# Kernel optimization log

Measured on AMD Instinct MI355X. Metric: run time of the kernel, lower is better.

The kernel has to match this reference:

```python
import jax, jax.numpy as jnp
import numpy as np

WS = 4            # window_size
C = 192           # dim
NH = 6            # num_heads
HD = C // NH      # head_dim
HID = 384         # mlp hidden = int(dim * mlp_ratio)
EPS = 1e-5


def _rel_pos_index(ws):
    coords = np.stack(np.meshgrid(np.arange(ws), np.arange(ws), np.arange(ws), indexing='ij'))  # [3,ws,ws,ws]
    cf = coords.reshape(3, -1)                                # [3, N]
    rel = cf[:, :, None] - cf[:, None, :]                     # [3, N, N]
    rel = rel.transpose(1, 2, 0)                              # [N, N, 3]
    rel += ws - 1
    rel[:, :, 0] *= (2 * ws - 1) * (2 * ws - 1)
    rel[:, :, 1] *= 2 * ws - 1
    return jnp.asarray(rel.sum(-1), dtype=jnp.int32)          # [N, N]

REL_IDX = _rel_pos_index(WS)


def setup_inputs() -> dict:
    key = jax.random.key(0)
    ks = jax.random.split(key, 20)
    s = 0.02
    B, Dd, Hh, Ww = 2, 48, 48, 48
    L = Dd * Hh * Ww
    tbl = (2 * WS - 1) ** 3
    return {
        'x': jax.random.normal(ks[0], (B, L, C), jnp.float32),
        'D': Dd, 'H': Hh, 'W': Ww,
        'ln1_g': jnp.ones((C,), jnp.float32), 'ln1_b': jnp.zeros((C,), jnp.float32),
        'ln2_g': jnp.ones((C,), jnp.float32), 'ln2_b': jnp.zeros((C,), jnp.float32),
        'qkv_w': jax.random.normal(ks[1], (C, 3 * C), jnp.float32) * s,
        'qkv_b': jnp.zeros((3 * C,), jnp.float32),
        'rpb_table': jax.random.normal(ks[2], (tbl, NH), jnp.float32) * s,
        'proj_w': jax.random.normal(ks[3], (C, C), jnp.float32) * s,
        'proj_b': jnp.zeros((C,), jnp.float32),
        'fc1_w': jax.random.normal(ks[4], (C, HID), jnp.float32) * s,
        'fc1_b': jnp.zeros((HID,), jnp.float32),
        'dw_w': jax.random.normal(ks[5], (HID, 1, 3, 3, 3), jnp.float32) * s,
        'dw_b': jnp.zeros((HID,), jnp.float32),
        'bn_g': jnp.ones((HID,), jnp.float32), 'bn_b': jnp.zeros((HID,), jnp.float32),
        'bn_mean': jnp.zeros((HID,), jnp.float32), 'bn_var': jnp.ones((HID,), jnp.float32),
        'fc2_w': jax.random.normal(ks[6], (HID, C), jnp.float32) * s,
        'fc2_b': jnp.zeros((C,), jnp.float32),
    }


def _ln(x, g, b):
    m = jnp.mean(x, -1, keepdims=True)
    v = jnp.mean((x - m) ** 2, -1, keepdims=True)
    return (x - m) * jax.lax.rsqrt(v + EPS) * g + b


def _window_attn(xw, qkv_w, qkv_b, rpb_table, proj_w, proj_b):
    # xw: [nW, N, C]
    nW, N, _ = xw.shape
    qkv = (xw @ qkv_w + qkv_b).reshape(nW, N, 3, NH, HD)
    q, k, v = qkv[:, :, 0], qkv[:, :, 1], qkv[:, :, 2]   # [nW, N, NH, HD]
    scale = HD ** -0.5
    attn = jnp.einsum('wnhd,wmhd->whnm', q * scale, k)    # [nW, NH, N, N]
    bias = rpb_table[REL_IDX]                              # [N, N, NH]
    attn = attn + jnp.transpose(bias, (2, 0, 1))[None]
    attn = jax.nn.softmax(attn, axis=-1)
    out = jnp.einsum('whnm,wmhd->wnhd', attn, v).reshape(nW, N, C)
    return out @ proj_w + proj_b


def reference(x, D, H, W, ln1_g, ln1_b, ln2_g, ln2_b, qkv_w, qkv_b, rpb_table,
              proj_w, proj_b, fc1_w, fc1_b, dw_w, dw_b, bn_g, bn_b, bn_mean,
              bn_var, fc2_w, fc2_b):
    B, L, _ = x.shape
    shortcut = x
    # --- windowed attention ---
    xs = _ln(x, ln1_g, ln1_b).reshape(B, D, H, W, C)
    # D,H,W divisible by WS -> no padding
    xs = xs.reshape(B, D // WS, WS, H // WS, WS, W // WS, WS, C)
    xw = jnp.transpose(xs, (0, 1, 3, 5, 2, 4, 6, 7)).reshape(-1, WS ** 3, C)
    aw = _window_attn(xw, qkv_w, qkv_b, rpb_table, proj_w, proj_b)
    aw = aw.reshape(B, D // WS, H // WS, W // WS, WS, WS, WS, C)
    xr = jnp.transpose(aw, (0, 1, 4, 2, 5, 3, 6, 7)).reshape(B, L, C)
    x = shortcut + xr
    # --- efficient MLP: fc1 -> dwconv3d -> BN(eval) -> GELU -> fc2 ---
    y = _ln(x, ln2_g, ln2_b)
    h = y @ fc1_w + fc1_b                                  # [B, L, HID]
    hs = jnp.transpose(h, (0, 2, 1)).reshape(B, HID, D, H, W)
    hs = jax.lax.conv_general_dilated(
        hs, dw_w, window_strides=(1, 1, 1), padding='SAME',
        feature_group_count=HID,
        dimension_numbers=('NCDHW', 'OIDHW', 'NCDHW')) + dw_b[None, :, None, None, None]
    hs = (hs - bn_mean[None, :, None, None, None]) * jax.lax.rsqrt(
        bn_var[None, :, None, None, None] + EPS) * bn_g[None, :, None, None, None] + bn_b[None, :, None, None, None]
    h = jnp.transpose(hs.reshape(B, HID, L), (0, 2, 1))
    h = jax.nn.gelu(h, approximate=False)
    return x + (h @ fc2_w + fc2_b)
```

## Files before the change

kernel.cpp:

```cpp
#include <hip/hip_runtime.h>

typedef __bf16 bf16;
typedef __bf16 bf16x8 __attribute__((ext_vector_type(8)));
typedef float f32x4 __attribute__((ext_vector_type(4)));
typedef float f32x2 __attribute__((ext_vector_type(2)));

#define L_TOT 110592
#define TOKS  221184
#define NWIN  3456

static __device__ __forceinline__ f32x4 mfma16(bf16x8 a, bf16x8 b, f32x4 c) {
    return __builtin_amdgcn_mfma_f32_16x16x32_bf16(a, b, c, 0, 0, 0);
}
static __device__ __forceinline__ bf16x8 ld8(const bf16* p) { return *(const bf16x8*)p; }
static __device__ __forceinline__ f32x2 pkfma(float w, f32x2 v, f32x2 c) {
    return __builtin_elementwise_fma((f32x2){w, w}, v, c);
}

__global__ void wt_frag(const float* __restrict__ src, bf16* __restrict__ dst, int K, int N) {
    int i = blockIdx.x * 256 + threadIdx.x;
    if (i >= K * N) return;
    int kw = i & 31, col = (i >> 5) & 63, rest = i >> 11;
    int nks = K >> 5;
    int ks = rest % nks, chunk = rest / nks;
    int n = chunk * 64 + col, k = ks * 32 + kw;
    dst[i] = (bf16)src[k * N + n];
}

__global__ void bias6_build(const float* __restrict__ rpb, float* __restrict__ bias6) {
    int i = blockIdx.x * 256 + threadIdx.x;
    if (i >= 6 * 64 * 64) return;
    int h = i >> 12, n = (i >> 6) & 63, m = i & 63;
    int r0 = (n >> 4) - (m >> 4) + 3;
    int r1 = ((n >> 2) & 3) - ((m >> 2) & 3) + 3;
    int r2 = (n & 3) - (m & 3) + 3;
    bias6[i] = rpb[(r0 * 49 + r1 * 7 + r2) * 6 + h];
}

__global__ void ln1_window(const float* __restrict__ x, const float* __restrict__ g,
                           const float* __restrict__ bt, bf16* __restrict__ xw) {
    int wave = threadIdx.x >> 6, lane = threadIdx.x & 63;
    int t = blockIdx.x * 4 + wave;
    const float* row = x + (long)t * 192;
    float v0 = row[lane], v1 = row[lane + 64], v2 = row[lane + 128];
    float s = v0 + v1 + v2;
    #pragma unroll
    for (int m = 1; m < 64; m <<= 1) s += __shfl_xor(s, m);
    float mu = s * (1.0f / 192.0f);
    float d0 = v0 - mu, d1 = v1 - mu, d2 = v2 - mu;
    float q = d0 * d0 + d1 * d1 + d2 * d2;
    #pragma unroll
    for (int m = 1; m < 64; m <<= 1) q += __shfl_xor(q, m);
    float r = rsqrtf(q * (1.0f / 192.0f) + 1e-5f);
    int b = t / L_TOT, l = t - b * L_TOT;
    int dz = l / 2304, rem = l - dz * 2304;
    int hy = rem / 48, wx = rem - hy * 48;
    int w = ((b * 12 + (dz >> 2)) * 12 + (hy >> 2)) * 12 + (wx >> 2);
    int n = (dz & 3) * 16 + (hy & 3) * 4 + (wx & 3);
    bf16* o = xw + (long)w * 12288 + (lane >> 5) * 2048 + n * 32 + (lane & 31);
    o[0]    = (bf16)(d0 * r * g[lane]       + bt[lane]);
    o[4096] = (bf16)(d1 * r * g[lane + 64]  + bt[lane + 64]);
    o[8192] = (bf16)(d2 * r * g[lane + 128] + bt[lane + 128]);
}

__global__ void ln2_kernel(const bf16* __restrict__ in, const float* __restrict__ g,
                           const float* __restrict__ bt, bf16* __restrict__ y) {
    int wave = threadIdx.x >> 6, lane = threadIdx.x & 63;
    long t = blockIdx.x * 4 + wave;
    const bf16* row = in + t * 192;
    float v0 = (float)row[lane], v1 = (float)row[lane + 64], v2 = (float)row[lane + 128];
    float s = v0 + v1 + v2;
    #pragma unroll
    for (int m = 1; m < 64; m <<= 1) s += __shfl_xor(s, m);
    float mu = s * (1.0f / 192.0f);
    float d0 = v0 - mu, d1 = v1 - mu, d2 = v2 - mu;
    float q = d0 * d0 + d1 * d1 + d2 * d2;
    #pragma unroll
    for (int m = 1; m < 64; m <<= 1) q += __shfl_xor(q, m);
    float r = rsqrtf(q * (1.0f / 192.0f) + 1e-5f);
    bf16* o = y + (t >> 6) * 12288 + (lane >> 5) * 2048 + (t & 63) * 32 + (lane & 31);
    o[0]    = (bf16)(d0 * r * g[lane]       + bt[lane]);
    o[4096] = (bf16)(d1 * r * g[lane + 64]  + bt[lane + 64]);
    o[8192] = (bf16)(d2 * r * g[lane + 128] + bt[lane + 128]);
}

__global__ __launch_bounds__(256) void gemm_qkv(
    const bf16* __restrict__ xw, const bf16* __restrict__ wt,
    const float* __restrict__ bqkv,
    bf16* __restrict__ qb, bf16* __restrict__ kb_, bf16* __restrict__ vtb) {
    int m0 = blockIdx.x * 128;
    int w0 = m0 >> 6;
    int wid = threadIdx.x >> 6, lane = threadIdx.x & 63;
    int wr = wid >> 1, wc = wid & 1;
    int lo = lane & 15, hi = lane >> 4;
    f32x4 zf = {0.f, 0.f, 0.f, 0.f};

    const bf16* Ab = xw + (long)(w0 + wr) * 12288 + (lo * 32 + hi * 8);
    bf16x8 a[4][6];
    #pragma unroll
    for (int ti = 0; ti < 4; ++ti)
        #pragma unroll
        for (int ks = 0; ks < 6; ++ks)
            a[ti][ks] = ld8(Ab + ks * 2048 + ti * 512);

    #pragma unroll
    for (int nc = 0; nc < 9; ++nc) {
        int sect = nc / 3;
        int cb0 = (nc - sect * 3) * 64;
        f32x4 acc[4][2];
        #pragma unroll
        for (int i = 0; i < 4; ++i) { acc[i][0] = zf; acc[i][1] = zf; }
        const bf16* Bb = wt + (long)nc * 12288 + (wc * 32 + lo) * 32 + hi * 8;
        #pragma unroll
        for (int ks = 0; ks < 6; ++ks) {
            bf16x8 b0 = ld8(Bb + ks * 2048);
            bf16x8 b1 = ld8(Bb + ks * 2048 + 512);
            #pragma unroll
            for (int ti = 0; ti < 4; ++ti) {
                acc[ti][0] = mfma16(a[ti][ks], b0, acc[ti][0]);
                acc[ti][1] = mfma16(a[ti][ks], b1, acc[ti][1]);
            }
        }
        #pragma unroll
        for (int ti = 0; ti < 4; ++ti)
            #pragma unroll
            for (int j = 0; j < 4; ++j) {
                int trow = m0 + wr * 64 + ti * 16 + hi * 4 + j;
                int w = trow >> 6, n = trow & 63;
                #pragma unroll
                for (int tj = 0; tj < 2; ++tj) {
                    int cw = cb0 + wc * 32 + tj * 16 + lo;
                    int h = cw >> 5, d = cw & 31;
                    float val = acc[ti][tj][j] + bqkv[sect * 192 + cw];
                    long wh = (long)(w * 6 + h);
                    if (sect == 0)       qb[(wh * 64 + n) * 32 + d] = (bf16)(val * 0.17677669529663687f);
                    else if (sect == 1)  kb_[(wh * 64 + n) * 32 + d] = (bf16)val;
                    else                 vtb[(wh * 32 + d) * 64 + n] = (bf16)val;
                }
            }
    }
}

__global__ __launch_bounds__(384) void attn_light(
    const bf16* __restrict__ qb, const bf16* __restrict__ kb_,
    const bf16* __restrict__ vtb, const float* __restrict__ bias6,
    bf16* __restrict__ aw) {
    __shared__ char p_smem[6 * 8192];
    int w = blockIdx.x;
    int h = threadIdx.x >> 6;
    int lane = threadIdx.x & 63;
    int lo = lane & 15, hi = lane >> 4;
    char* ph = p_smem + h * 8192;
    long wh = (long)(w * 6 + h);
    f32x4 zf = {0.f, 0.f, 0.f, 0.f};

    bf16x8 qa[4], kb[4];
    #pragma unroll
    for (int ti = 0; ti < 4; ++ti) qa[ti] = ld8(qb  + (wh * 64 + ti * 16 + lo) * 32 + hi * 8);
    #pragma unroll
    for (int tj = 0; tj < 4; ++tj) kb[tj] = ld8(kb_ + (wh * 64 + tj * 16 + lo) * 32 + hi * 8);
    f32x4 s[4][4];
    #pragma unroll
    for (int ti = 0; ti < 4; ++ti)
        #pragma unroll
        for (int tj = 0; tj < 4; ++tj)
            s[ti][tj] = mfma16(qa[ti], kb[tj], zf);

    const float* bh = bias6 + h * 4096;
    #pragma unroll
    for (int ti = 0; ti < 4; ++ti)
        #pragma unroll
        for (int j = 0; j < 4; ++j) {
            int rr = ti * 16 + hi * 4 + j;
            float ev[4];
            #pragma unroll
            for (int tj = 0; tj < 4; ++tj) s[ti][tj][j] += bh[rr * 64 + tj * 16 + lo];
            float mx = fmaxf(fmaxf(s[ti][0][j], s[ti][1][j]), fmaxf(s[ti][2][j], s[ti][3][j]));
            #pragma unroll
            for (int m = 1; m < 16; m <<= 1) mx = fmaxf(mx, __shfl_xor(mx, m));
            float sum = 0.f;
            #pragma unroll
            for (int tj = 0; tj < 4; ++tj) { ev[tj] = __expf(s[ti][tj][j] - mx); sum += ev[tj]; }
            #pragma unroll
            for (int m = 1; m < 16; m <<= 1) sum += __shfl_xor(sum, m);
            float inv = 1.0f / sum;
            #pragma unroll
            for (int tj = 0; tj < 4; ++tj) {
                int byte = ((rr * 64 + tj * 16 + lo) * 2) ^ ((rr & 7) << 4);
                *(bf16*)(ph + byte) = (bf16)(ev[tj] * inv);
            }
        }

    f32x4 o[4][2];
    #pragma unroll
    for (int i = 0; i < 4; ++i) { o[i][0] = zf; o[i][1] = zf; }
    #pragma unroll
    for (int ks2 = 0; ks2 < 2; ++ks2) {
        bf16x8 pa[4], vb[2];
        #pragma unroll
        for (int ti = 0; ti < 4; ++ti) {
            int row = ti * 16 + lo;
            pa[ti] = *(const bf16x8*)(ph + ((row * 128 + ks2 * 64 + hi * 16) ^ ((row & 7) << 4)));
        }
        #pragma unroll
        for (int td = 0; td < 2; ++td)
            vb[td] = ld8(vtb + (wh * 32 + td * 16 + lo) * 64 + ks2 * 32 + hi * 8);
        #pragma unroll
        for (int ti = 0; ti < 4; ++ti)
            #pragma unroll
            for (int td = 0; td < 2; ++td)
                o[ti][td] = mfma16(pa[ti], vb[td], o[ti][td]);
    }
    bf16* orow = aw + wh * 2048;
    #pragma unroll
    for (int ti = 0; ti < 4; ++ti)
        #pragma unroll
        for (int td = 0; td < 2; ++td)
            #pragma unroll
            for (int j = 0; j < 4; ++j)
                orow[(ti * 16 + hi * 4 + j) * 32 + td * 16 + lo] = (bf16)o[ti][td][j];
}

__global__ __launch_bounds__(256) void gemm_proj(
    const bf16* __restrict__ aw, const bf16* __restrict__ wt,
    const float* __restrict__ bias, const float* __restrict__ x,
    bf16* __restrict__ out1) {
    int m0 = blockIdx.x * 128;
    int w0 = m0 >> 6;
    int wid = threadIdx.x >> 6, lane = threadIdx.x & 63;
    int wr = wid >> 1, wc = wid & 1;
    int lo = lane & 15, hi = lane >> 4;
    f32x4 zf = {0.f, 0.f, 0.f, 0.f};

    const bf16* Ab = aw + (long)(w0 + wr) * 12288 + (lo * 32 + hi * 8);
    bf16x8 a[4][6];
    #pragma unroll
    for (int ti = 0; ti < 4; ++ti)
        #pragma unroll
        for (int ks = 0; ks < 6; ++ks)
            a[ti][ks] = ld8(Ab + ks * 2048 + ti * 512);

    #pragma unroll
    for (int nc = 0; nc < 3; ++nc) {
        f32x4 acc[4][2];
        #pragma unroll
        for (int i = 0; i < 4; ++i) { acc[i][0] = zf; acc[i][1] = zf; }
        const bf16* Bb = wt + (long)nc * 12288 + (wc * 32 + lo) * 32 + hi * 8;
        #pragma unroll
        for (int ks = 0; ks < 6; ++ks) {
            bf16x8 b0 = ld8(Bb + ks * 2048);
            bf16x8 b1 = ld8(Bb + ks * 2048 + 512);
            #pragma unroll
            for (int ti = 0; ti < 4; ++ti) {
                acc[ti][0] = mfma16(a[ti][ks], b0, acc[ti][0]);
                acc[ti][1] = mfma16(a[ti][ks], b1, acc[ti][1]);
            }
        }
        #pragma unroll
        for (int ti = 0; ti < 4; ++ti)
            #pragma unroll
            for (int j = 0; j < 4; ++j) {
                int trow = m0 + wr * 64 + ti * 16 + hi * 4 + j;
                int wv = trow >> 6, n = trow & 63;
                int bb = wv / 1728; int rem = wv - bb * 1728;
                int dq = rem / 144; int rem2 = rem - dq * 144;
                int hq = rem2 / 12; int wq = rem2 - hq * 12;
                int l = (dq * 4 + (n >> 4)) * 2304 + (hq * 4 + ((n >> 2) & 3)) * 48 + (wq * 4 + (n & 3));
                long base = ((long)bb * L_TOT + l) * 192;
                #pragma unroll
                for (int tj = 0; tj < 2; ++tj) {
                    int col = nc * 64 + wc * 32 + tj * 16 + lo;
                    out1[base + col] = (bf16)(x[base + col] + acc[ti][tj][j] + bias[col]);
                }
            }
    }
}

__global__ __launch_bounds__(256) void gemm_fc1(
    const bf16* __restrict__ y, const bf16* __restrict__ wt,
    const float* __restrict__ bias, bf16* __restrict__ h_t) {
    __shared__ bf16 tl[64][136];
    int m0 = blockIdx.x * 128;
    int c0 = m0 >> 6;
    int wid = threadIdx.x >> 6, lane = threadIdx.x & 63;
    int wr = wid >> 1, wc = wid & 1;
    int lo = lane & 15, hi = lane >> 4;
    f32x4 zf = {0.f, 0.f, 0.f, 0.f};
    int bb = m0 / L_TOT; int l0 = m0 - bb * L_TOT;
    int col = threadIdx.x >> 2, seg = threadIdx.x & 3;

    const bf16* Ab = y + (long)(c0 + wr) * 12288 + (lo * 32 + hi * 8);
    bf16x8 a[4][6];
    #pragma unroll
    for (int ti = 0; ti < 4; ++ti)
        #pragma unroll
        for (int ks = 0; ks < 6; ++ks)
            a[ti][ks] = ld8(Ab + ks * 2048 + ti * 512);

    #pragma unroll
    for (int nc = 0; nc < 6; ++nc) {
        f32x4 acc[4][2];
        #pragma unroll
        for (int i = 0; i < 4; ++i) { acc[i][0] = zf; acc[i][1] = zf; }
        const bf16* Bb = wt + (long)nc * 12288 + (wc * 32 + lo) * 32 + hi * 8;
        #pragma unroll
        for (int ks = 0; ks < 6; ++ks) {
            bf16x8 b0 = ld8(Bb + ks * 2048);
            bf16x8 b1 = ld8(Bb + ks * 2048 + 512);
            #pragma unroll
            for (int ti = 0; ti < 4; ++ti) {
                acc[ti][0] = mfma16(a[ti][ks], b0, acc[ti][0]);
                acc[ti][1] = mfma16(a[ti][ks], b1, acc[ti][1]);
            }
        }
        if (nc) __syncthreads();
        #pragma unroll
        for (int ti = 0; ti < 4; ++ti)
            #pragma unroll
            for (int tj = 0; tj < 2; ++tj)
                #pragma unroll
                for (int j = 0; j < 4; ++j) {
                    int rl = wr * 64 + ti * 16 + hi * 4 + j;
                    int cl = wc * 32 + tj * 16 + lo;
                    tl[cl][rl] = (bf16)(acc[ti][tj][j] + bias[nc * 64 + cl]);
                }
        __syncthreads();
        bf16* dst = h_t + ((long)bb * 384 + nc * 64 + col) * L_TOT + l0 + seg * 32;
        #pragma unroll
        for (int i8 = 0; i8 < 4; ++i8)
            *(bf16x8*)(dst + i8 * 8) = *(const bf16x8*)(&tl[col][seg * 32 + i8 * 8]);
    }
}

__global__ __launch_bounds__(320) void dwconv_bn_gelu(
    const bf16* __restrict__ h_t, const float* __restrict__ wconv,
    const float* __restrict__ cb, const float* __restrict__ bng,
    const float* __restrict__ bnb, const float* __restrict__ bnm,
    const float* __restrict__ bnv, bf16* __restrict__ g_t) {
    __shared__ __align__(16) bf16 tile[289 * 56];
    int blk = blockIdx.x;
    int bb = blk / 4608; int rem = blk - bb * 4608;
    int ch = rem / 12; int zb = rem - ch * 12; int z0 = zb * 4;
    const bf16* src = h_t + ((long)bb * 384 + ch) * L_TOT;

    uint4 zv = make_uint4(0u, 0u, 0u, 0u);
    for (int i = threadIdx.x; i < 295; i += 320) {
        int e = (i < 7) ? i * 8 : ((i - 7 + 1) * 56 + 48);
        *(uint4*)(tile + e) = zv;
    }
    for (int c = threadIdx.x; c < 1728; c += 320) {
        int zi = c / 288; int rc = c - zi * 288;
        int r = rc / 6; int cx8 = rc - r * 6;
        int gz = z0 - 1 + zi;
        uint4 val = zv;
        if (gz >= 0 && gz < 48) val = *(const uint4*)(src + (long)gz * 2304 + r * 48 + cx8 * 8);
        *(uint4*)(tile + (1 + zi * 48 + r) * 56 + cx8 * 8) = val;
    }
    float wgt[27];
    #pragma unroll
    for (int i = 0; i < 27; ++i) wgt[i] = wconv[ch * 27 + i];
    float scale = bng[ch] * rsqrtf(bnv[ch] + 1e-5f);
    float shift = bnb[ch] - bnm[ch] * scale;
    float cbias = cb[ch];
    __syncthreads();

    if (threadIdx.x < 288) {
        int y = threadIdx.x / 6, cx = threadIdx.x - y * 6, x0 = cx * 8;
        __builtin_assume(y < 48);
        bool up_ok = (y > 0), dn_ok = (y < 47);
        bf16* dstc = g_t + ((long)bb * 384 + ch) * L_TOT + (long)z0 * 2304 + y * 48 + x0;
        f32x2 accp[4][4];
        #pragma unroll
        for (int p = 0; p < 4; ++p)
            #pragma unroll
            for (int i = 0; i < 4; ++i) accp[p][i] = (f32x2){0.f, 0.f};

        #pragma unroll
        for (int zi = 0; zi < 6; ++zi) {
            const bf16* plane = tile + (1 + zi * 48) * 56;
            #pragma unroll
            for (int dy = 0; dy < 3; ++dy) {
                bool ok = (dy == 1) || (dy == 0 ? up_ok : dn_ok);
                if (ok) {
                    const bf16* rp = plane + (y + dy - 1) * 56 + x0;
                    bf16x8 mv = ld8(rp);
                    float d[8];
                    #pragma unroll
                    for (int i = 0; i < 8; ++i) d[i] = (float)mv[i];
                    float hl = (float)rp[-1];
                    float hr = (float)rp[8];
                    f32x2 E[5], O[4];
                    E[0] = (f32x2){hl,  d[0]};
                    E[1] = (f32x2){d[1], d[2]};
                    E[2] = (f32x2){d[3], d[4]};
                    E[3] = (f32x2){d[5], d[6]};
                    E[4] = (f32x2){d[7], hr};
                    O[0] = (f32x2){d[0], d[1]};
                    O[1] = (f32x2){d[2], d[3]};
                    O[2] = (f32x2){d[4], d[5]};
                    O[3] = (f32x2){d[6], d[7]};
                    #pragma unroll
                    for (int dz = 0; dz < 3; ++dz) {
                        int p = zi - dz;
                        if (p >= 0 && p <= 3) {
                            float w0 = wgt[dz * 9 + dy * 3 + 0];
                            float w1 = wgt[dz * 9 + dy * 3 + 1];
                            float w2 = wgt[dz * 9 + dy * 3 + 2];
                            #pragma unroll
                            for (int i = 0; i < 4; ++i)
                                accp[p][i] = pkfma(w0, E[i], pkfma(w1, O[i], pkfma(w2, E[i + 1], accp[p][i])));
                        }
                    }
                }
            }
            if (zi >= 2) {
                int p = zi - 2;
                bf16x8 ov;
                #pragma unroll
                for (int k = 0; k < 8; ++k) {
                    float v = accp[p][k >> 1][k & 1] + cbias;
                    v = fmaf(v, scale, shift);
                    float v2 = v * v;
                    float u2 = v * fmaf(v2, 0.0713548162726f, 1.5957691216057308f);
                    float e  = __expf(u2);
                    float q  = __builtin_amdgcn_rcpf(e + 1.0f);
                    ov[k] = (bf16)(v - v * q);
                }
                *(bf16x8*)(dstc + p * 2304) = ov;
            }
        }
    }
}

__global__ __launch_bounds__(256) void gemm_fc2(
    const bf16* __restrict__ g_t, const bf16* __restrict__ wt,
    const float* __restrict__ bias, const bf16* __restrict__ out1,
    float* __restrict__ out) {
    __shared__ bf16 As[2][4096];
    int m0 = blockIdx.x * 64;
    int wc = threadIdx.x >> 6, lane = threadIdx.x & 63;
    int lo = lane & 15, hi = lane >> 4;
    int bb = m0 / L_TOT, l0 = m0 - bb * L_TOT;
    f32x4 zf = {0.f, 0.f, 0.f, 0.f};
    f32x4 acc[3][4];
    #pragma unroll
    for (int tj = 0; tj < 3; ++tj)
        #pragma unroll
        for (int ti = 0; ti < 4; ++ti) acc[tj][ti] = zf;

    int sch = threadIdx.x >> 3;
    int seg = threadIdx.x & 7;
    const bf16* srcb = g_t + ((long)bb * 384 + sch) * L_TOT + l0 + seg * 8;

    bf16x8 r[2][2];
    #pragma unroll
    for (int p = 0; p < 2; ++p) r[0][p] = ld8(srcb + (long)(p * 32) * L_TOT);
    #pragma unroll
    for (int p = 0; p < 2; ++p)
        #pragma unroll
        for (int i = 0; i < 8; ++i)
            As[0][(seg * 8 + i) * 64 + ((p * 32 + sch) ^ (((seg ^ i) & 7) << 3))] = r[0][p][i];
    #pragma unroll
    for (int p = 0; p < 2; ++p) r[0][p] = ld8(srcb + (long)(64 + p * 32) * L_TOT);
    #pragma unroll
    for (int p = 0; p < 2; ++p) r[1][p] = ld8(srcb + (long)(128 + p * 32) * L_TOT);

    float res[3][4][4];
    #pragma unroll
    for (int tj = 0; tj < 3; ++tj)
        #pragma unroll
        for (int ti = 0; ti < 4; ++ti)
            #pragma unroll
            for (int j = 0; j < 4; ++j) {
                long trow = m0 + ti * 16 + hi * 4 + j;
                res[tj][ti][j] = (float)out1[trow * 192 + wc * 48 + tj * 16 + lo];
            }
    __syncthreads();

    #pragma unroll
    for (int t = 0; t < 6; ++t) {
        const bf16* Ac = As[t & 1];
        #pragma unroll
        for (int ksin = 0; ksin < 2; ++ksin) {
            bf16x8 a[4];
            #pragma unroll
            for (int ti = 0; ti < 4; ++ti) {
                int rr = ti * 16 + lo;
                int S = ((rr >> 3) ^ rr) & 7;
                a[ti] = *(const bf16x8*)&Ac[rr * 64 + ((ksin * 32 + hi * 8) ^ (S << 3))];
            }
            #pragma unroll
            for (int tj = 0; tj < 3; ++tj) {
                int cstart = wc * 48 + tj * 16;
                bf16x8 b0 = ld8(wt + ((long)((cstart >> 6) * 12 + t * 2 + ksin) * 64 + (cstart & 63) + lo) * 32 + hi * 8);
                #pragma unroll
                for (int ti = 0; ti < 4; ++ti)
                    acc[tj][ti] = mfma16(a[ti], b0, acc[tj][ti]);
            }
        }
        if (t < 5) {
            bf16* An = As[(t + 1) & 1];
            #pragma unroll
            for (int p = 0; p < 2; ++p)
                #pragma unroll
                for (int i = 0; i < 8; ++i)
                    An[(seg * 8 + i) * 64 + ((p * 32 + sch) ^ (((seg ^ i) & 7) << 3))] = r[t & 1][p][i];
        }
        if (t < 3) {
            #pragma unroll
            for (int p = 0; p < 2; ++p)
                r[t & 1][p] = ld8(srcb + (long)((t + 3) * 64 + p * 32) * L_TOT);
        }
        __syncthreads();
    }
    #pragma unroll
    for (int tj = 0; tj < 3; ++tj)
        #pragma unroll
        for (int ti = 0; ti < 4; ++ti)
            #pragma unroll
            for (int j = 0; j < 4; ++j) {
                long trow = m0 + ti * 16 + hi * 4 + j;
                int col = wc * 48 + tj * 16 + lo;
                out[trow * 192 + col] = res[tj][ti][j] + acc[tj][ti][j] + bias[col];
            }
}

extern "C" void kernel_launch(void* const* d_in, const int* in_sizes, int n_in,
                              void* d_out, int out_size, void* d_ws, size_t ws_size,
                              hipStream_t stream) {
    (void)in_sizes; (void)n_in; (void)out_size; (void)ws_size;
    const float* x     = (const float*)d_in[0];
    const float* ln1g  = (const float*)d_in[4];
    const float* ln1b  = (const float*)d_in[5];
    const float* ln2g  = (const float*)d_in[6];
    const float* ln2b  = (const float*)d_in[7];
    const float* qkvw  = (const float*)d_in[8];
    const float* qkvb  = (const float*)d_in[9];
    const float* rpb   = (const float*)d_in[10];
    const float* projw = (const float*)d_in[11];
    const float* projb = (const float*)d_in[12];
    const float* fc1w  = (const float*)d_in[13];
    const float* fc1b  = (const float*)d_in[14];
    const float* dww   = (const float*)d_in[15];
    const float* dwb   = (const float*)d_in[16];
    const float* bng   = (const float*)d_in[17];
    const float* bnb   = (const float*)d_in[18];
    const float* bnm   = (const float*)d_in[19];
    const float* bnv   = (const float*)d_in[20];
    const float* fc2w  = (const float*)d_in[21];
    const float* fc2b  = (const float*)d_in[22];
    float* out = (float*)d_out;

    char* ws = (char*)d_ws;
    size_t o = 0;
    bf16*  out1 = (bf16*)(ws + o);
    bf16*  vt_buf = (bf16*)(ws + o + 84934656); o += 169869312;
    bf16*  h_t  = (bf16*)(ws + o); o += 169869312;
    bf16*  region1 = (bf16*)(ws + o); o += 169869312;
    bf16*  xw  = region1;
    bf16*  aw  = region1 + 42467328;
    bf16*  yb  = region1;
    bf16*  g_t = region1;
    bf16*  qkvwt  = (bf16*)(ws + o); o += 221184;
    bf16*  projwt = (bf16*)(ws + o); o += 73728;
    bf16*  fc1wt  = (bf16*)(ws + o); o += 147456;
    bf16*  fc2wt  = (bf16*)(ws + o); o += 147456;
    float* bias6  = (float*)(ws + o); o += 98304;

    bf16* q_buf  = h_t;
    bf16* k_buf  = h_t + 42467328;

    wt_frag<<<(110592 + 255) / 256, 256, 0, stream>>>(qkvw, qkvwt, 192, 576);
    wt_frag<<<(36864 + 255) / 256, 256, 0, stream>>>(projw, projwt, 192, 192);
    wt_frag<<<(73728 + 255) / 256, 256, 0, stream>>>(fc1w, fc1wt, 192, 384);
    wt_frag<<<(73728 + 255) / 256, 256, 0, stream>>>(fc2w, fc2wt, 384, 192);
    bias6_build<<<96, 256, 0, stream>>>(rpb, bias6);

    ln1_window<<<55296, 256, 0, stream>>>(x, ln1g, ln1b, xw);
    gemm_qkv<<<1728, 256, 0, stream>>>(xw, qkvwt, qkvb, q_buf, k_buf, vt_buf);
    attn_light<<<NWIN, 384, 0, stream>>>(q_buf, k_buf, vt_buf, bias6, aw);
    gemm_proj<<<1728, 256, 0, stream>>>(aw, projwt, projb, x, out1);
    ln2_kernel<<<55296, 256, 0, stream>>>(out1, ln2g, ln2b, yb);
    gemm_fc1<<<1728, 256, 0, stream>>>(yb, fc1wt, fc1b, h_t);
    dwconv_bn_gelu<<<9216, 320, 0, stream>>>(h_t, dww, dwb, bng, bnb, bnm, bnv, g_t);
    gemm_fc2<<<3456, 256, 0, stream>>>(g_t, fc2wt, fc2b, out1, out);
}
```

Measured before the change: 739.7 us.

## Pad dwconv smem rows to 60, load per-thread rows, use scalar FMAs

The depthwise conv kernel's shared tile row stride changes from 56 to 60 bf16 elements, with reads and writes split into 8-byte halves, presumably to reduce LDS bank conflicts. The tile is now filled so each active thread loads its own row segment for all six z planes, and only the halo words are zeroed. Packed f32x2 FMAs are replaced by scalar fmaf over a 10-element window, which removes the register shuffling that built the packed pairs but may issue more instructions. The GELU sigmoid's constants are pre-scaled by log2(e) so exp2f can replace __expf.

```diff
diff --git a/kernel.cpp b/kernel.cpp
--- a/kernel.cpp
+++ b/kernel.cpp
@@ -2,8 +2,8 @@
 
 typedef __bf16 bf16;
 typedef __bf16 bf16x8 __attribute__((ext_vector_type(8)));
+typedef __bf16 bf16x4 __attribute__((ext_vector_type(4)));
 typedef float f32x4 __attribute__((ext_vector_type(4)));
-typedef float f32x2 __attribute__((ext_vector_type(2)));
 
 #define L_TOT 110592
 #define TOKS  221184
@@ -13,9 +13,6 @@
     return __builtin_amdgcn_mfma_f32_16x16x32_bf16(a, b, c, 0, 0, 0);
 }
 static __device__ __forceinline__ bf16x8 ld8(const bf16* p) { return *(const bf16x8*)p; }
-static __device__ __forceinline__ f32x2 pkfma(float w, f32x2 v, f32x2 c) {
-    return __builtin_elementwise_fma((f32x2){w, w}, v, c);
-}
 
 __global__ void wt_frag(const float* __restrict__ src, bf16* __restrict__ dst, int K, int N) {
     int i = blockIdx.x * 256 + threadIdx.x;
@@ -337,24 +334,31 @@
     const float* __restrict__ cb, const float* __restrict__ bng,
     const float* __restrict__ bnb, const float* __restrict__ bnm,
     const float* __restrict__ bnv, bf16* __restrict__ g_t) {
-    __shared__ __align__(16) bf16 tile[289 * 56];
+    __shared__ __align__(16) bf16 tile[289 * 60];
     int blk = blockIdx.x;
     int bb = blk / 4608; int rem = blk - bb * 4608;
     int ch = rem / 12; int zb = rem - ch * 12; int z0 = zb * 4;
     const bf16* src = h_t + ((long)bb * 384 + ch) * L_TOT;
 
-    uint4 zv = make_uint4(0u, 0u, 0u, 0u);
-    for (int i = threadIdx.x; i < 295; i += 320) {
-        int e = (i < 7) ? i * 8 : ((i - 7 + 1) * 56 + 48);
-        *(uint4*)(tile + e) = zv;
-    }
-    for (int c = threadIdx.x; c < 1728; c += 320) {
-        int zi = c / 288; int rc = c - zi * 288;
-        int r = rc / 6; int cx8 = rc - r * 6;
-        int gz = z0 - 1 + zi;
-        uint4 val = zv;
-        if (gz >= 0 && gz < 48) val = *(const uint4*)(src + (long)gz * 2304 + r * 48 + cx8 * 8);
-        *(uint4*)(tile + (1 + zi * 48 + r) * 56 + cx8 * 8) = val;
+    int y = threadIdx.x / 6, cx = threadIdx.x - y * 6, x0 = cx * 8;
+    bool active = threadIdx.x < 288;
+
+    uint2 z2 = make_uint2(0u, 0u);
+    for (int i = threadIdx.x; i < 15; i += 320) *(uint2*)(tile + i * 4) = z2;
+    for (int i = threadIdx.x; i < 576; i += 320) {
+        int r = (i >> 1) + 1;
+        *(unsigned*)(tile + r * 60 + ((i & 1) ? 58 : 48)) = 0u;
+    }
+    if (active) {
+        #pragma unroll
+        for (int zi = 0; zi < 6; ++zi) {
+            int gz = z0 - 1 + zi;
+            uint4 val = make_uint4(0u, 0u, 0u, 0u);
+            if (gz >= 0 && gz < 48) val = *(const uint4*)(src + (long)gz * 2304 + y * 48 + x0);
+            bf16* dst = tile + (1 + zi * 48 + y) * 60 + x0;
+            *(uint2*)(dst)     = make_uint2(val.x, val.y);
+            *(uint2*)(dst + 4) = make_uint2(val.z, val.w);
+        }
     }
     float wgt[27];
     #pragma unroll
@@ -364,41 +368,31 @@
     float cbias = cb[ch];
     __syncthreads();
 
-    if (threadIdx.x < 288) {
-        int y = threadIdx.x / 6, cx = threadIdx.x - y * 6, x0 = cx * 8;
+    if (active) {
         __builtin_assume(y < 48);
         bool up_ok = (y > 0), dn_ok = (y < 47);
         bf16* dstc = g_t + ((long)bb * 384 + ch) * L_TOT + (long)z0 * 2304 + y * 48 + x0;
-        f32x2 accp[4][4];
+        float acc[4][8];
         #pragma unroll
         for (int p = 0; p < 4; ++p)
             #pragma unroll
-            for (int i = 0; i < 4; ++i) accp[p][i] = (f32x2){0.f, 0.f};
+            for (int k = 0; k < 8; ++k) acc[p][k] = 0.f;
 
         #pragma unroll
         for (int zi = 0; zi < 6; ++zi) {
-            const bf16* plane = tile + (1 + zi * 48) * 56;
+            const bf16* plane = tile + (1 + zi * 48) * 60;
             #pragma unroll
             for (int dy = 0; dy < 3; ++dy) {
                 bool ok = (dy == 1) || (dy == 0 ? up_ok : dn_ok);
                 if (ok) {
-                    const bf16* rp = plane + (y + dy - 1) * 56 + x0;
-                    bf16x8 mv = ld8(rp);
-                    float d[8];
+                    const bf16* rp = plane + (y + dy - 1) * 60 + x0;
+                    bf16x4 mlo = *(const bf16x4*)rp;
+                    bf16x4 mhi = *(const bf16x4*)(rp + 4);
+                    float s[10];
+                    s[0] = (float)rp[-1];
                     #pragma unroll
-                    for (int i = 0; i < 8; ++i) d[i] = (float)mv[i];
-                    float hl = (float)rp[-1];
-                    float hr = (float)rp[8];
-                    f32x2 E[5], O[4];
-                    E[0] = (f32x2){hl,  d[0]};
-                    E[1] = (f32x2){d[1], d[2]};
-                    E[2] = (f32x2){d[3], d[4]};
-                    E[3] = (f32x2){d[5], d[6]};
-                    E[4] = (f32x2){d[7], hr};
-                    O[0] = (f32x2){d[0], d[1]};
-                    O[1] = (f32x2){d[2], d[3]};
-                    O[2] = (f32x2){d[4], d[5]};
-                    O[3] = (f32x2){d[6], d[7]};
+                    for (int i = 0; i < 4; ++i) { s[1 + i] = (float)mlo[i]; s[5 + i] = (float)mhi[i]; }
+                    s[9] = (float)rp[8];
                     #pragma unroll
                     for (int dz = 0; dz < 3; ++dz) {
                         int p = zi - dz;
@@ -407,8 +401,8 @@
                             float w1 = wgt[dz * 9 + dy * 3 + 1];
                             float w2 = wgt[dz * 9 + dy * 3 + 2];
                             #pragma unroll
-                            for (int i = 0; i < 4; ++i)
-                                accp[p][i] = pkfma(w0, E[i], pkfma(w1, O[i], pkfma(w2, E[i + 1], accp[p][i])));
+                            for (int k = 0; k < 8; ++k)
+                                acc[p][k] = fmaf(w0, s[k], fmaf(w1, s[k + 1], fmaf(w2, s[k + 2], acc[p][k])));
                         }
                     }
                 }
@@ -418,11 +412,11 @@
                 bf16x8 ov;
                 #pragma unroll
                 for (int k = 0; k < 8; ++k) {
-                    float v = accp[p][k >> 1][k & 1] + cbias;
+                    float v = acc[p][k] + cbias;
                     v = fmaf(v, scale, shift);
                     float v2 = v * v;
-                    float u2 = v * fmaf(v2, 0.0713548162726f, 1.5957691216057308f);
-                    float e  = __expf(u2);
+                    float u2 = v * fmaf(v2, 0.10294357f, 2.3022080918f);
+                    float e  = exp2f(u2);
                     float q  = __builtin_amdgcn_rcpf(e + 1.0f);
                     ov[k] = (bf16)(v - v * q);
                 }
```

New measurement: 755.3 us. 2.1% more time.
